# Performance work log

Hardware: AMD Instinct MI355X
Metric: run time of the kernel (lower is better)

Reference implementation:

```python
import jax, jax.numpy as jnp
import numpy as np

B, S, DIM, H = 2, 2048, 1024, 16
HD = DIM // H

def setup_inputs() -> dict:
    key = jax.random.key(0)
    ks = jax.random.split(key, 11)
    sc = DIM ** -0.5
    return {
        "q": jax.random.normal(ks[0], (B, S, DIM), jnp.float32),
        "k": jax.random.normal(ks[1], (B, S, DIM), jnp.float32),
        "v": jax.random.normal(ks[2], (B, S, DIM), jnp.float32),
        "Wq": jax.random.normal(ks[3], (DIM, DIM), jnp.float32) * sc,
        "bq": jax.random.normal(ks[4], (DIM,), jnp.float32) * 0.02,
        "Wk": jax.random.normal(ks[5], (DIM, DIM), jnp.float32) * sc,
        "bk": jax.random.normal(ks[6], (DIM,), jnp.float32) * 0.02,
        "Wv": jax.random.normal(ks[7], (DIM, DIM), jnp.float32) * sc,
        "bv": jax.random.normal(ks[8], (DIM,), jnp.float32) * 0.02,
        "Wo": jax.random.normal(ks[9], (DIM, DIM), jnp.float32) * sc,
        "bo": jax.random.normal(ks[10], (DIM,), jnp.float32) * 0.02,
    }

def reference(q, k, v, Wq, bq, Wk, bk, Wv, bv, Wo, bo):
    b, s, _ = q.shape
    qh = (q @ Wq + bq).reshape(b, s, H, HD).transpose(0, 2, 1, 3)  # [B,H,S,HD]
    kh = (k @ Wk + bk).reshape(b, s, H, HD).transpose(0, 2, 1, 3)
    vh = (v @ Wv + bv).reshape(b, s, H, HD).transpose(0, 2, 1, 3)
    scale = HD ** -0.5
    scores = jnp.einsum('bhqd,bhkd->bhqk', qh, kh) * scale  # [B,H,S,S]
    causal = jnp.triu(jnp.ones((s, s), dtype=bool), k=1)
    scores = jnp.where(causal, -jnp.inf, scores)
    attn = jax.nn.softmax(scores, axis=-1)
    out = jnp.einsum('bhqk,bhkd->bhqd', attn, vh)
    out = out.transpose(0, 2, 1, 3).reshape(b, s, DIM)
    return out @ Wo + bo
```

## Files before the change

kernel.cpp:

```cpp
#include <hip/hip_runtime.h>

#define DIM 1024
#define SEQ 2048
#define NH 16
#define HD 64
#define M_TOT 4096

typedef unsigned short u16;
typedef unsigned int u32;
typedef __attribute__((ext_vector_type(8))) short bf16x8;
typedef __attribute__((ext_vector_type(4))) float f32x4;
typedef __attribute__((ext_vector_type(4))) u32 u32x4;
typedef __attribute__((ext_vector_type(4))) u16 u16x4;

__device__ __forceinline__ u16 f2bf(float f) {
  u32 x = __builtin_bit_cast(u32, f);
  x = x + 0x7fffu + ((x >> 16) & 1u);
  return (u16)(x >> 16);
}
__device__ __forceinline__ void gload_lds16(const void* g, void* l) {
  __builtin_amdgcn_global_load_lds(
      (const __attribute__((address_space(1))) u32*)g,
      (__attribute__((address_space(3))) u32*)l, 16, 0, 0);
}

__global__ __launch_bounds__(256)
void zero_out_k(u32* __restrict__ o, int n)
{
  int i = blockIdx.x * 256 + threadIdx.x;
  if (i < n) o[i] = 0;
}

__global__ __launch_bounds__(256)
void transpose_weights(const float* __restrict__ w0, const float* __restrict__ w1,
                       const float* __restrict__ w2, const float* __restrict__ w3,
                       u16* __restrict__ wt)
{
  __shared__ u16 tile[64][72];
  int z = blockIdx.z;
  const float* W = z == 0 ? w0 : z == 1 ? w1 : z == 2 ? w2 : w3;
  u16* Wt = wt + (size_t)z * DIM * DIM;
  int k0 = blockIdx.x * 64, n0 = blockIdx.y * 64;
  int t = threadIdx.x;
#pragma unroll
  for (int it = 0; it < 4; ++it) {
    int idx = it * 256 + t;
    int lr = idx >> 4, c0 = (idx & 15) * 4;
    f32x4 v = *(const f32x4*)&W[(size_t)(k0 + lr) * DIM + n0 + c0];
    u16x4 h;
#pragma unroll
    for (int j = 0; j < 4; ++j) h[j] = f2bf(v[j]);
    *(u16x4*)&tile[lr][c0] = h;
  }
  __syncthreads();
#pragma unroll
  for (int it = 0; it < 2; ++it) {
    int idx = it * 256 + t;
    int nr = idx >> 3, c0 = (idx & 7) * 8;
    alignas(16) u16 tmp[8];
#pragma unroll
    for (int j = 0; j < 8; ++j) tmp[j] = tile[c0 + j][nr];
    *(u32x4*)&Wt[(size_t)(n0 + nr) * DIM + k0 + c0] = *(u32x4*)tmp;
  }
}

#define BM 128
#define BN 128
#define BK 32

template <bool AF32, bool OUTF32>
__device__ __forceinline__ void gemm_tile(
    const void* __restrict__ Xv, const u16* __restrict__ Wt,
    const float* __restrict__ bias, void* __restrict__ Yv,
    int bm, int bn)
{
  __shared__ u16 lA[BM * BK];
  __shared__ u16 lB[BN * BK];
  int t = threadIdx.x;
  int lane = t & 63, w = t >> 6;
  int wr = (w >> 1) * 64, wc = (w & 1) * 64;
  int rl = lane & 15, kb = (lane >> 4) * 8;

  f32x4 acc[4][4] = {};

  for (int k0 = 0; k0 < DIM; k0 += BK) {
    if (AF32) {
      const float* Xf = (const float*)Xv;
#pragma unroll
      for (int it = 0; it < 4; ++it) {
        int idx = it * 256 + t;
        int row = idx >> 3, c4 = (idx & 7) * 4;
        f32x4 v = *(const f32x4*)&Xf[(size_t)(bm + row) * DIM + k0 + c4];
        u16x4 h;
#pragma unroll
        for (int j = 0; j < 4; ++j) h[j] = f2bf(v[j]);
        *(u16x4*)&lA[row * BK + c4] = h;
      }
    } else {
      const u16* Xh = (const u16*)Xv;
#pragma unroll
      for (int r = 0; r < 2; ++r) {
        int idx = r * 256 + t;
        int row = idx >> 2, ce = (idx & 3) * 8;
        gload_lds16(Xh + (size_t)(bm + row) * DIM + k0 + ce, (char*)lA + idx * 16);
      }
    }
#pragma unroll
    for (int r = 0; r < 2; ++r) {
      int idx = r * 256 + t;
      int row = idx >> 2, ce = (idx & 3) * 8;
      gload_lds16(Wt + (size_t)(bn + row) * DIM + k0 + ce, (char*)lB + idx * 16);
    }
    __syncthreads();
    bf16x8 a[4], b[4];
#pragma unroll
    for (int m = 0; m < 4; ++m)
      a[m] = *(const bf16x8*)&lA[(wr + m * 16 + rl) * BK + kb];
#pragma unroll
    for (int n = 0; n < 4; ++n)
      b[n] = *(const bf16x8*)&lB[(wc + n * 16 + rl) * BK + kb];
#pragma unroll
    for (int m = 0; m < 4; ++m)
#pragma unroll
      for (int n = 0; n < 4; ++n)
        acc[m][n] = __builtin_amdgcn_mfma_f32_16x16x32_bf16(a[m], b[n], acc[m][n], 0, 0, 0);
    __syncthreads();
  }

  int rh = (lane >> 4) * 4;
#pragma unroll
  for (int n = 0; n < 4; ++n) {
    int col = bn + wc + n * 16 + rl;
    float bv = bias[col];
#pragma unroll
    for (int m = 0; m < 4; ++m) {
      int row = bm + wr + m * 16 + rh;
#pragma unroll
      for (int r = 0; r < 4; ++r) {
        if (OUTF32)
          ((float*)Yv)[(size_t)(row + r) * DIM + col] = acc[m][n][r] + bv;
        else
          ((u16*)Yv)[(size_t)(row + r) * DIM + col] = f2bf(acc[m][n][r] + bv);
      }
    }
  }
}

__global__ __launch_bounds__(256)
void gemm_qkv(const float* __restrict__ xq, const float* __restrict__ xk, const float* __restrict__ xv,
              const u16* __restrict__ wt,
              const float* __restrict__ bq, const float* __restrict__ bk, const float* __restrict__ bv,
              u16* __restrict__ outbase)
{
  int z = blockIdx.z;
  const float* X = z == 0 ? xq : z == 1 ? xk : xv;
  const u16* Wt = wt + (size_t)z * DIM * DIM;
  const float* bias = z == 0 ? bq : z == 1 ? bk : bv;
  u16* Y = outbase + (size_t)z * M_TOT * DIM;
  gemm_tile<true, false>(X, Wt, bias, Y, blockIdx.x * BM, blockIdx.y * BN);
}

__global__ __launch_bounds__(256)
void gemm_o(const u16* __restrict__ X, const u16* __restrict__ Wt,
            const float* __restrict__ bias, float* __restrict__ Y)
{
  gemm_tile<false, true>(X, Wt, bias, Y, blockIdx.x * BM, blockIdx.y * BN);
}

#define SC2 0.18033688011112042f

__device__ __forceinline__ void attn_compute(
    const u16 (*lK)[72], const u16 (*lVt)[72], u16 (*lPw)[72],
    bf16x8 qf0, bf16x8 qf1, bf16x8 ones,
    int rl, int hi, int kv0, int qw, bool diag,
    f32x4* oacc, f32x4& lacc)
{
  float p[4][4];
#pragma unroll
  for (int g = 0; g < 4; ++g) {
    int kvr = g * 16 + rl;
    f32x4 c = {};
    c = __builtin_amdgcn_mfma_f32_16x16x32_bf16(qf0, *(const bf16x8*)&lK[kvr][hi * 8], c, 0, 0, 0);
    c = __builtin_amdgcn_mfma_f32_16x16x32_bf16(qf1, *(const bf16x8*)&lK[kvr][32 + hi * 8], c, 0, 0, 0);
#pragma unroll
    for (int r = 0; r < 4; ++r) p[g][r] = exp2f(c[r] * SC2);
  }
  if (diag) {
#pragma unroll
    for (int g = 0; g < 4; ++g) {
      int kv_abs = kv0 + g * 16 + rl;
#pragma unroll
      for (int r = 0; r < 4; ++r)
        if (kv_abs > qw + hi * 4 + r) p[g][r] = 0.f;
    }
  }
#pragma unroll
  for (int g = 0; g < 4; ++g)
#pragma unroll
    for (int r = 0; r < 4; ++r)
      lPw[hi * 4 + r][g * 16 + rl] = f2bf(p[g][r]);
#pragma unroll
  for (int kk = 0; kk < 2; ++kk) {
    bf16x8 pf = *(const bf16x8*)&lPw[rl][kk * 32 + hi * 8];
    lacc = __builtin_amdgcn_mfma_f32_16x16x32_bf16(pf, ones, lacc, 0, 0, 0);
#pragma unroll
    for (int n = 0; n < 4; ++n) {
      bf16x8 vf = *(const bf16x8*)&lVt[n * 16 + rl][kk * 32 + hi * 8];
      oacc[n] = __builtin_amdgcn_mfma_f32_16x16x32_bf16(pf, vf, oacc[n], 0, 0, 0);
    }
  }
}

__global__ __launch_bounds__(256)
void attn_fwd(const u16* Qp, const u16* __restrict__ Kp,
              const u16* __restrict__ Vp, u16* O)
{
  __shared__ u16 lK[64][72];
  __shared__ u16 lVt[64][72];
  __shared__ u16 lP[4][16][72];

  int bh = blockIdx.y;
  int b = bh >> 4, h = bh & 15;
  int xa = blockIdx.x;
  int xb = 31 - xa;
  int t = threadIdx.x, lane = t & 63, w = t >> 6;
  int rl = lane & 15, hi = lane >> 4;
  int qa_w = xa * 64 + w * 16;
  int qb_w = xb * 64 + w * 16;

  const u16* Qb = Qp + ((size_t)b * SEQ) * DIM + h * HD;
  const u16* Kb = Kp + ((size_t)b * SEQ) * DIM + h * HD;
  const u16* Vb = Vp + ((size_t)b * SEQ) * DIM + h * HD;

  bf16x8 qa0, qa1, qb0, qb1;
  {
    const u16* qrow = Qb + (size_t)(qa_w + rl) * DIM + hi * 8;
    qa0 = *(const bf16x8*)qrow;
    qa1 = *(const bf16x8*)(qrow + 32);
    qrow = Qb + (size_t)(qb_w + rl) * DIM + hi * 8;
    qb0 = *(const bf16x8*)qrow;
    qb1 = *(const bf16x8*)(qrow + 32);
  }
  bf16x8 ones;
#pragma unroll
  for (int j = 0; j < 8; ++j) ones[j] = (short)0x3F80;

  f32x4 oA[4] = {}, oB[4] = {};
  f32x4 lAcc = {}, lBcc = {};

  int krow = t >> 3;
  int kc8 = (t & 7) * 8;
  int kvv = t & 63;
  int vd0 = (t >> 6) * 8;

  int nt = xb + 1;
  bf16x8 kr0, kr1, vr0, vr1;
  {
    const u16* Krow = Kb + kc8;
    kr0 = *(const bf16x8*)(Krow + (size_t)krow * DIM);
    kr1 = *(const bf16x8*)(Krow + (size_t)(krow + 32) * DIM);
    const u16* Vrow = Vb + (size_t)kvv * DIM + vd0;
    vr0 = *(const bf16x8*)Vrow;
    vr1 = *(const bf16x8*)(Vrow + 32);
  }

  for (int tile = 0; tile < nt; ++tile) {
    *(bf16x8*)&lK[krow][kc8] = kr0;
    *(bf16x8*)&lK[krow + 32][kc8] = kr1;
#pragma unroll
    for (int j = 0; j < 8; ++j) lVt[vd0 + j][kvv] = (u16)vr0[j];
#pragma unroll
    for (int j = 0; j < 8; ++j) lVt[vd0 + 32 + j][kvv] = (u16)vr1[j];
    __syncthreads();
    if (tile + 1 < nt) {
      size_t kv0n = (size_t)(tile + 1) * 64;
      const u16* Krow = Kb + kv0n * DIM + kc8;
      kr0 = *(const bf16x8*)(Krow + (size_t)krow * DIM);
      kr1 = *(const bf16x8*)(Krow + (size_t)(krow + 32) * DIM);
      const u16* Vrow = Vb + (kv0n + kvv) * DIM + vd0;
      vr0 = *(const bf16x8*)Vrow;
      vr1 = *(const bf16x8*)(Vrow + 32);
    }
    int kv0 = tile * 64;
    attn_compute(lK, lVt, lP[w], qb0, qb1, ones, rl, hi, kv0, qb_w, tile == xb, oB, lBcc);
    if (tile <= xa)
      attn_compute(lK, lVt, lP[w], qa0, qa1, ones, rl, hi, kv0, qa_w, tile == xa, oA, lAcc);
    __syncthreads();
  }

#pragma unroll
  for (int n = 0; n < 4; ++n) {
    int d = n * 16 + rl;
#pragma unroll
    for (int r = 0; r < 4; ++r) {
      int qq = qa_w + hi * 4 + r;
      O[((size_t)b * SEQ + qq) * DIM + h * HD + d] = f2bf(oA[n][r] / lAcc[r]);
      qq = qb_w + hi * 4 + r;
      O[((size_t)b * SEQ + qq) * DIM + h * HD + d] = f2bf(oB[n][r] / lBcc[r]);
    }
  }
}

extern "C" void kernel_launch(void* const* d_in, const int* in_sizes, int n_in,
                              void* d_out, int out_size, void* d_ws, size_t ws_size,
                              hipStream_t stream)
{
  (void)in_sizes; (void)n_in;
  const size_t MB = 1024ull * 1024ull;
  if (ws_size < 32 * MB) {
    zero_out_k<<<(out_size + 255) / 256, 256, 0, stream>>>((u32*)d_out, out_size);
    return;
  }

  u16* Wt = (u16*)d_ws;
  u16* Qp = (u16*)((char*)d_ws + 8 * MB);
  u16* Kp = (u16*)((char*)d_ws + 16 * MB);
  u16* Vp = (u16*)((char*)d_ws + 24 * MB);

  transpose_weights<<<dim3(16, 16, 4), 256, 0, stream>>>(
      (const float*)d_in[3], (const float*)d_in[5], (const float*)d_in[7],
      (const float*)d_in[9], Wt);
  gemm_qkv<<<dim3(32, 8, 3), 256, 0, stream>>>(
      (const float*)d_in[0], (const float*)d_in[1], (const float*)d_in[2], Wt,
      (const float*)d_in[4], (const float*)d_in[6], (const float*)d_in[8], Qp);
  attn_fwd<<<dim3(16, 32), 256, 0, stream>>>(Qp, Kp, Vp, Qp);
  gemm_o<<<dim3(32, 8), 256, 0, stream>>>(Qp, Wt + 3ll * DIM * DIM,
                                          (const float*)d_in[10], (float*)d_out);
}
```

Baseline: 133.1 us.

## Double-buffer GEMM tiles and interleave dual-query attention compute

The projection GEMM now double-buffers its LDS tiles and prefetches the next K-slice (including register-staged fp32 activations) during the MFMA work on the current slice. This drops one barrier per iteration. The attention kernel adds a fused dual-query path that shares the K/V fragment loads between the two query tiles and interleaves their MFMAs for more instruction-level parallelism. It also sets an occupancy hint of 2 blocks per CU. The costs are double the GEMM LDS footprint, more registers in the dual path, and the occupancy bound may force register spills.

```diff
diff --git a/kernel.cpp b/kernel.cpp
--- a/kernel.cpp
+++ b/kernel.cpp
@@ -74,57 +74,98 @@
     const float* __restrict__ bias, void* __restrict__ Yv,
     int bm, int bn)
 {
-  __shared__ u16 lA[BM * BK];
-  __shared__ u16 lB[BN * BK];
+  __shared__ u16 lA[2][BM * BK];
+  __shared__ u16 lB[2][BN * BK];
   int t = threadIdx.x;
   int lane = t & 63, w = t >> 6;
   int wr = (w >> 1) * 64, wc = (w & 1) * 64;
   int rl = lane & 15, kb = (lane >> 4) * 8;
 
+  const float* Xf = (const float*)Xv;
+  const u16* Xh = (const u16*)Xv;
+
   f32x4 acc[4][4] = {};
-
-  for (int k0 = 0; k0 < DIM; k0 += BK) {
-    if (AF32) {
-      const float* Xf = (const float*)Xv;
+  f32x4 av[4];
+
+  if (AF32) {
+#pragma unroll
+    for (int it = 0; it < 4; ++it) {
+      int idx = it * 256 + t;
+      int row = idx >> 3, c4 = (idx & 7) * 4;
+      f32x4 v = *(const f32x4*)&Xf[(size_t)(bm + row) * DIM + c4];
+      u16x4 h;
+#pragma unroll
+      for (int j = 0; j < 4; ++j) h[j] = f2bf(v[j]);
+      *(u16x4*)&lA[0][row * BK + c4] = h;
+    }
+  } else {
+#pragma unroll
+    for (int r = 0; r < 2; ++r) {
+      int idx = r * 256 + t;
+      int row = idx >> 2, ce = (idx & 3) * 8;
+      gload_lds16(Xh + (size_t)(bm + row) * DIM + ce, (char*)&lA[0][0] + idx * 16);
+    }
+  }
+#pragma unroll
+  for (int r = 0; r < 2; ++r) {
+    int idx = r * 256 + t;
+    int row = idx >> 2, ce = (idx & 3) * 8;
+    gload_lds16(Wt + (size_t)(bn + row) * DIM + ce, (char*)&lB[0][0] + idx * 16);
+  }
+
+  for (int ki = 0; ki < DIM / BK; ++ki) {
+    int cur = ki & 1, nxt = cur ^ 1;
+    __syncthreads();
+    int k1 = (ki + 1) * BK;
+    bool more = k1 < DIM;
+    if (more) {
+      if (AF32) {
+#pragma unroll
+        for (int it = 0; it < 4; ++it) {
+          int idx = it * 256 + t;
+          int row = idx >> 3, c4 = (idx & 7) * 4;
+          av[it] = *(const f32x4*)&Xf[(size_t)(bm + row) * DIM + k1 + c4];
+        }
+      } else {
+#pragma unroll
+        for (int r = 0; r < 2; ++r) {
+          int idx = r * 256 + t;
+          int row = idx >> 2, ce = (idx & 3) * 8;
+          gload_lds16(Xh + (size_t)(bm + row) * DIM + k1 + ce,
+                      (char*)&lA[nxt][0] + idx * 16);
+        }
+      }
+#pragma unroll
+      for (int r = 0; r < 2; ++r) {
+        int idx = r * 256 + t;
+        int row = idx >> 2, ce = (idx & 3) * 8;
+        gload_lds16(Wt + (size_t)(bn + row) * DIM + k1 + ce,
+                    (char*)&lB[nxt][0] + idx * 16);
+      }
+    }
+    bf16x8 a[4], b[4];
+#pragma unroll
+    for (int m = 0; m < 4; ++m)
+      a[m] = *(const bf16x8*)&lA[cur][(wr + m * 16 + rl) * BK + kb];
+#pragma unroll
+    for (int n = 0; n < 4; ++n)
+      b[n] = *(const bf16x8*)&lB[cur][(wc + n * 16 + rl) * BK + kb];
+#pragma unroll
+    for (int m = 0; m < 4; ++m)
+#pragma unroll
+      for (int n = 0; n < 4; ++n)
+        acc[m][n] = __builtin_amdgcn_mfma_f32_16x16x32_bf16(a[m], b[n], acc[m][n], 0, 0, 0);
+    if (more && AF32) {
 #pragma unroll
       for (int it = 0; it < 4; ++it) {
         int idx = it * 256 + t;
         int row = idx >> 3, c4 = (idx & 7) * 4;
-        f32x4 v = *(const f32x4*)&Xf[(size_t)(bm + row) * DIM + k0 + c4];
         u16x4 h;
 #pragma unroll
-        for (int j = 0; j < 4; ++j) h[j] = f2bf(v[j]);
-        *(u16x4*)&lA[row * BK + c4] = h;
+        for (int j = 0; j < 4; ++j) h[j] = f2bf(av[it][j]);
+        *(u16x4*)&lA[nxt][row * BK + c4] = h;
       }
-    } else {
-      const u16* Xh = (const u16*)Xv;
-#pragma unroll
-      for (int r = 0; r < 2; ++r) {
-        int idx = r * 256 + t;
-        int row = idx >> 2, ce = (idx & 3) * 8;
-        gload_lds16(Xh + (size_t)(bm + row) * DIM + k0 + ce, (char*)lA + idx * 16);
-      }
-    }
-#pragma unroll
-    for (int r = 0; r < 2; ++r) {
-      int idx = r * 256 + t;
-      int row = idx >> 2, ce = (idx & 3) * 8;
-      gload_lds16(Wt + (size_t)(bn + row) * DIM + k0 + ce, (char*)lB + idx * 16);
-    }
-    __syncthreads();
-    bf16x8 a[4], b[4];
-#pragma unroll
-    for (int m = 0; m < 4; ++m)
-      a[m] = *(const bf16x8*)&lA[(wr + m * 16 + rl) * BK + kb];
-#pragma unroll
-    for (int n = 0; n < 4; ++n)
-      b[n] = *(const bf16x8*)&lB[(wc + n * 16 + rl) * BK + kb];
-#pragma unroll
-    for (int m = 0; m < 4; ++m)
-#pragma unroll
-      for (int n = 0; n < 4; ++n)
-        acc[m][n] = __builtin_amdgcn_mfma_f32_16x16x32_bf16(a[m], b[n], acc[m][n], 0, 0, 0);
-    __syncthreads();
+    }
   }
 
   int rh = (lane >> 4) * 4;
@@ -211,13 +252,68 @@
   }
 }
 
-__global__ __launch_bounds__(256)
+__device__ __forceinline__ void attn_compute_dual(
+    const u16 (*lK)[72], const u16 (*lVt)[72],
+    u16 (*lP0)[72], u16 (*lP1)[72],
+    bf16x8 qa0, bf16x8 qa1, bf16x8 qb0, bf16x8 qb1, bf16x8 ones,
+    int rl, int hi, int kv0, int qaw, bool diagA,
+    f32x4* oA, f32x4& lA, f32x4* oB, f32x4& lB)
+{
+  float pA[4][4], pB[4][4];
+#pragma unroll
+  for (int g = 0; g < 4; ++g) {
+    int kvr = g * 16 + rl;
+    bf16x8 kf0 = *(const bf16x8*)&lK[kvr][hi * 8];
+    bf16x8 kf1 = *(const bf16x8*)&lK[kvr][32 + hi * 8];
+    f32x4 cA = {}, cB = {};
+    cA = __builtin_amdgcn_mfma_f32_16x16x32_bf16(qa0, kf0, cA, 0, 0, 0);
+    cB = __builtin_amdgcn_mfma_f32_16x16x32_bf16(qb0, kf0, cB, 0, 0, 0);
+    cA = __builtin_amdgcn_mfma_f32_16x16x32_bf16(qa1, kf1, cA, 0, 0, 0);
+    cB = __builtin_amdgcn_mfma_f32_16x16x32_bf16(qb1, kf1, cB, 0, 0, 0);
+#pragma unroll
+    for (int r = 0; r < 4; ++r) {
+      pA[g][r] = exp2f(cA[r] * SC2);
+      pB[g][r] = exp2f(cB[r] * SC2);
+    }
+  }
+  if (diagA) {
+#pragma unroll
+    for (int g = 0; g < 4; ++g) {
+      int kv_abs = kv0 + g * 16 + rl;
+#pragma unroll
+      for (int r = 0; r < 4; ++r)
+        if (kv_abs > qaw + hi * 4 + r) pA[g][r] = 0.f;
+    }
+  }
+#pragma unroll
+  for (int g = 0; g < 4; ++g)
+#pragma unroll
+    for (int r = 0; r < 4; ++r) {
+      lP0[hi * 4 + r][g * 16 + rl] = f2bf(pA[g][r]);
+      lP1[hi * 4 + r][g * 16 + rl] = f2bf(pB[g][r]);
+    }
+#pragma unroll
+  for (int kk = 0; kk < 2; ++kk) {
+    bf16x8 pfA = *(const bf16x8*)&lP0[rl][kk * 32 + hi * 8];
+    bf16x8 pfB = *(const bf16x8*)&lP1[rl][kk * 32 + hi * 8];
+    lA = __builtin_amdgcn_mfma_f32_16x16x32_bf16(pfA, ones, lA, 0, 0, 0);
+    lB = __builtin_amdgcn_mfma_f32_16x16x32_bf16(pfB, ones, lB, 0, 0, 0);
+#pragma unroll
+    for (int n = 0; n < 4; ++n) {
+      bf16x8 vf = *(const bf16x8*)&lVt[n * 16 + rl][kk * 32 + hi * 8];
+      oA[n] = __builtin_amdgcn_mfma_f32_16x16x32_bf16(pfA, vf, oA[n], 0, 0, 0);
+      oB[n] = __builtin_amdgcn_mfma_f32_16x16x32_bf16(pfB, vf, oB[n], 0, 0, 0);
+    }
+  }
+}
+
+__global__ __launch_bounds__(256, 2)
 void attn_fwd(const u16* Qp, const u16* __restrict__ Kp,
               const u16* __restrict__ Vp, u16* O)
 {
   __shared__ u16 lK[64][72];
   __shared__ u16 lVt[64][72];
-  __shared__ u16 lP[4][16][72];
+  __shared__ u16 lP[4][2][16][72];
 
   int bh = blockIdx.y;
   int b = bh >> 4, h = bh & 15;
@@ -282,9 +378,12 @@
       vr1 = *(const bf16x8*)(Vrow + 32);
     }
     int kv0 = tile * 64;
-    attn_compute(lK, lVt, lP[w], qb0, qb1, ones, rl, hi, kv0, qb_w, tile == xb, oB, lBcc);
     if (tile <= xa)
-      attn_compute(lK, lVt, lP[w], qa0, qa1, ones, rl, hi, kv0, qa_w, tile == xa, oA, lAcc);
+      attn_compute_dual(lK, lVt, lP[w][0], lP[w][1], qa0, qa1, qb0, qb1, ones,
+                        rl, hi, kv0, qa_w, tile == xa, oA, lAcc, oB, lBcc);
+    else
+      attn_compute(lK, lVt, lP[w][0], qb0, qb1, ones,
+                   rl, hi, kv0, qb_w, tile == xb, oB, lBcc);
     __syncthreads();
   }
 
```

After: 144.0 us. +8.2%, slower.

## Double-buffer GEMM tile loads in LDS to overlap loads with MFMA

Applied to the files above, without the earlier changes.

Switches the projection GEMM's LDS tiles to two buffers. The next K-slice is prefetched (global_load_lds for bf16 inputs, register loads for fp32 inputs) while MFMAs run on the current slice, and fp32 data is converted to bf16 and stored after the compute. This removes one barrier per iteration and hides global load latency. In exchange it doubles LDS use and adds registers for the prefetched fp32 values, which may lower occupancy.

```diff
diff --git a/kernel.cpp b/kernel.cpp
--- a/kernel.cpp
+++ b/kernel.cpp
@@ -74,57 +74,98 @@
     const float* __restrict__ bias, void* __restrict__ Yv,
     int bm, int bn)
 {
-  __shared__ u16 lA[BM * BK];
-  __shared__ u16 lB[BN * BK];
+  __shared__ u16 lA[2][BM * BK];
+  __shared__ u16 lB[2][BN * BK];
   int t = threadIdx.x;
   int lane = t & 63, w = t >> 6;
   int wr = (w >> 1) * 64, wc = (w & 1) * 64;
   int rl = lane & 15, kb = (lane >> 4) * 8;
 
+  const float* Xf = (const float*)Xv;
+  const u16* Xh = (const u16*)Xv;
+
   f32x4 acc[4][4] = {};
-
-  for (int k0 = 0; k0 < DIM; k0 += BK) {
-    if (AF32) {
-      const float* Xf = (const float*)Xv;
+  f32x4 av[4];
+
+  if (AF32) {
+#pragma unroll
+    for (int it = 0; it < 4; ++it) {
+      int idx = it * 256 + t;
+      int row = idx >> 3, c4 = (idx & 7) * 4;
+      f32x4 v = *(const f32x4*)&Xf[(size_t)(bm + row) * DIM + c4];
+      u16x4 h;
+#pragma unroll
+      for (int j = 0; j < 4; ++j) h[j] = f2bf(v[j]);
+      *(u16x4*)&lA[0][row * BK + c4] = h;
+    }
+  } else {
+#pragma unroll
+    for (int r = 0; r < 2; ++r) {
+      int idx = r * 256 + t;
+      int row = idx >> 2, ce = (idx & 3) * 8;
+      gload_lds16(Xh + (size_t)(bm + row) * DIM + ce, (char*)&lA[0][0] + idx * 16);
+    }
+  }
+#pragma unroll
+  for (int r = 0; r < 2; ++r) {
+    int idx = r * 256 + t;
+    int row = idx >> 2, ce = (idx & 3) * 8;
+    gload_lds16(Wt + (size_t)(bn + row) * DIM + ce, (char*)&lB[0][0] + idx * 16);
+  }
+
+  for (int ki = 0; ki < DIM / BK; ++ki) {
+    int cur = ki & 1, nxt = cur ^ 1;
+    __syncthreads();
+    int k1 = (ki + 1) * BK;
+    bool more = k1 < DIM;
+    if (more) {
+      if (AF32) {
+#pragma unroll
+        for (int it = 0; it < 4; ++it) {
+          int idx = it * 256 + t;
+          int row = idx >> 3, c4 = (idx & 7) * 4;
+          av[it] = *(const f32x4*)&Xf[(size_t)(bm + row) * DIM + k1 + c4];
+        }
+      } else {
+#pragma unroll
+        for (int r = 0; r < 2; ++r) {
+          int idx = r * 256 + t;
+          int row = idx >> 2, ce = (idx & 3) * 8;
+          gload_lds16(Xh + (size_t)(bm + row) * DIM + k1 + ce,
+                      (char*)&lA[nxt][0] + idx * 16);
+        }
+      }
+#pragma unroll
+      for (int r = 0; r < 2; ++r) {
+        int idx = r * 256 + t;
+        int row = idx >> 2, ce = (idx & 3) * 8;
+        gload_lds16(Wt + (size_t)(bn + row) * DIM + k1 + ce,
+                    (char*)&lB[nxt][0] + idx * 16);
+      }
+    }
+    bf16x8 a[4], b[4];
+#pragma unroll
+    for (int m = 0; m < 4; ++m)
+      a[m] = *(const bf16x8*)&lA[cur][(wr + m * 16 + rl) * BK + kb];
+#pragma unroll
+    for (int n = 0; n < 4; ++n)
+      b[n] = *(const bf16x8*)&lB[cur][(wc + n * 16 + rl) * BK + kb];
+#pragma unroll
+    for (int m = 0; m < 4; ++m)
+#pragma unroll
+      for (int n = 0; n < 4; ++n)
+        acc[m][n] = __builtin_amdgcn_mfma_f32_16x16x32_bf16(a[m], b[n], acc[m][n], 0, 0, 0);
+    if (more && AF32) {
 #pragma unroll
       for (int it = 0; it < 4; ++it) {
         int idx = it * 256 + t;
         int row = idx >> 3, c4 = (idx & 7) * 4;
-        f32x4 v = *(const f32x4*)&Xf[(size_t)(bm + row) * DIM + k0 + c4];
         u16x4 h;
 #pragma unroll
-        for (int j = 0; j < 4; ++j) h[j] = f2bf(v[j]);
-        *(u16x4*)&lA[row * BK + c4] = h;
+        for (int j = 0; j < 4; ++j) h[j] = f2bf(av[it][j]);
+        *(u16x4*)&lA[nxt][row * BK + c4] = h;
       }
-    } else {
-      const u16* Xh = (const u16*)Xv;
-#pragma unroll
-      for (int r = 0; r < 2; ++r) {
-        int idx = r * 256 + t;
-        int row = idx >> 2, ce = (idx & 3) * 8;
-        gload_lds16(Xh + (size_t)(bm + row) * DIM + k0 + ce, (char*)lA + idx * 16);
-      }
-    }
-#pragma unroll
-    for (int r = 0; r < 2; ++r) {
-      int idx = r * 256 + t;
-      int row = idx >> 2, ce = (idx & 3) * 8;
-      gload_lds16(Wt + (size_t)(bn + row) * DIM + k0 + ce, (char*)lB + idx * 16);
-    }
-    __syncthreads();
-    bf16x8 a[4], b[4];
-#pragma unroll
-    for (int m = 0; m < 4; ++m)
-      a[m] = *(const bf16x8*)&lA[(wr + m * 16 + rl) * BK + kb];
-#pragma unroll
-    for (int n = 0; n < 4; ++n)
-      b[n] = *(const bf16x8*)&lB[(wc + n * 16 + rl) * BK + kb];
-#pragma unroll
-    for (int m = 0; m < 4; ++m)
-#pragma unroll
-      for (int n = 0; n < 4; ++n)
-        acc[m][n] = __builtin_amdgcn_mfma_f32_16x16x32_bf16(a[m], b[n], acc[m][n], 0, 0, 0);
-    __syncthreads();
+    }
   }
 
   int rh = (lane >> 4) * 4;
```

After: 138.2 us. 3.8% more time.

## Switch attention to 32x32x16 MFMA with 32-row warp tiles and paired query blocks

Applied to the files above, without the earlier changes.

Rewrites the attention inner step to use 32x32x16 bf16 MFMAs, so each wave handles 32 query rows instead of 16. Each block now covers two near/far 64-row query tile pairs across its four waves, which halves the grid to 8x32 blocks and doubles how many query rows reuse each K/V tile staged in LDS. The aim is fewer K/V global loads and LDS fills per query row, plus better MFMA throughput. The cost is that waves in a block now have unequal tile counts, so some idle through the shared tile loop, and the grid has fewer blocks, which lowers occupancy and parallelism.

```diff
diff --git a/kernel.cpp b/kernel.cpp
--- a/kernel.cpp
+++ b/kernel.cpp
@@ -10,6 +10,7 @@
 typedef unsigned int u32;
 typedef __attribute__((ext_vector_type(8))) short bf16x8;
 typedef __attribute__((ext_vector_type(4))) float f32x4;
+typedef __attribute__((ext_vector_type(16))) float f32x16;
 typedef __attribute__((ext_vector_type(4))) u32 u32x4;
 typedef __attribute__((ext_vector_type(4))) u16 u16x4;
 
@@ -169,45 +170,41 @@
 
 #define SC2 0.18033688011112042f
 
-__device__ __forceinline__ void attn_compute(
+__device__ __forceinline__ void attn_compute32(
     const u16 (*lK)[72], const u16 (*lVt)[72], u16 (*lPw)[72],
-    bf16x8 qf0, bf16x8 qf1, bf16x8 ones,
-    int rl, int hi, int kv0, int qw, bool diag,
-    f32x4* oacc, f32x4& lacc)
-{
-  float p[4][4];
-#pragma unroll
-  for (int g = 0; g < 4; ++g) {
-    int kvr = g * 16 + rl;
-    f32x4 c = {};
-    c = __builtin_amdgcn_mfma_f32_16x16x32_bf16(qf0, *(const bf16x8*)&lK[kvr][hi * 8], c, 0, 0, 0);
-    c = __builtin_amdgcn_mfma_f32_16x16x32_bf16(qf1, *(const bf16x8*)&lK[kvr][32 + hi * 8], c, 0, 0, 0);
-#pragma unroll
-    for (int r = 0; r < 4; ++r) p[g][r] = exp2f(c[r] * SC2);
-  }
-  if (diag) {
-#pragma unroll
-    for (int g = 0; g < 4; ++g) {
-      int kv_abs = kv0 + g * 16 + rl;
-#pragma unroll
-      for (int r = 0; r < 4; ++r)
-        if (kv_abs > qw + hi * 4 + r) p[g][r] = 0.f;
-    }
-  }
-#pragma unroll
-  for (int g = 0; g < 4; ++g)
-#pragma unroll
-    for (int r = 0; r < 4; ++r)
-      lPw[hi * 4 + r][g * 16 + rl] = f2bf(p[g][r]);
-#pragma unroll
-  for (int kk = 0; kk < 2; ++kk) {
-    bf16x8 pf = *(const bf16x8*)&lPw[rl][kk * 32 + hi * 8];
-    lacc = __builtin_amdgcn_mfma_f32_16x16x32_bf16(pf, ones, lacc, 0, 0, 0);
-#pragma unroll
-    for (int n = 0; n < 4; ++n) {
-      bf16x8 vf = *(const bf16x8*)&lVt[n * 16 + rl][kk * 32 + hi * 8];
-      oacc[n] = __builtin_amdgcn_mfma_f32_16x16x32_bf16(pf, vf, oacc[n], 0, 0, 0);
-    }
+    const bf16x8* qf, bf16x8 ones,
+    int l31, int h5, int kv0, int qbase, bool diag,
+    f32x16& o0, f32x16& o1, f32x16& lacc)
+{
+  f32x16 sa = {}, sb = {};
+#pragma unroll
+  for (int ds = 0; ds < 4; ++ds) {
+    bf16x8 ka = *(const bf16x8*)&lK[l31][ds * 16 + h5 * 8];
+    bf16x8 kb = *(const bf16x8*)&lK[32 + l31][ds * 16 + h5 * 8];
+    sa = __builtin_amdgcn_mfma_f32_32x32x16_bf16(qf[ds], ka, sa, 0, 0, 0);
+    sb = __builtin_amdgcn_mfma_f32_32x32x16_bf16(qf[ds], kb, sb, 0, 0, 0);
+  }
+#pragma unroll
+  for (int r = 0; r < 16; ++r) {
+    int lq = (r & 3) + 8 * (r >> 2) + 4 * h5;
+    float pa = exp2f(sa[r] * SC2);
+    float pb = exp2f(sb[r] * SC2);
+    if (diag) {
+      int qrow = qbase + lq;
+      if (kv0 + l31 > qrow) pa = 0.f;
+      if (kv0 + 32 + l31 > qrow) pb = 0.f;
+    }
+    lPw[lq][l31] = f2bf(pa);
+    lPw[lq][32 + l31] = f2bf(pb);
+  }
+#pragma unroll
+  for (int ks = 0; ks < 4; ++ks) {
+    bf16x8 pf = *(const bf16x8*)&lPw[l31][ks * 16 + h5 * 8];
+    lacc = __builtin_amdgcn_mfma_f32_32x32x16_bf16(pf, ones, lacc, 0, 0, 0);
+    bf16x8 va = *(const bf16x8*)&lVt[l31][ks * 16 + h5 * 8];
+    bf16x8 vb = *(const bf16x8*)&lVt[32 + l31][ks * 16 + h5 * 8];
+    o0 = __builtin_amdgcn_mfma_f32_32x32x16_bf16(pf, va, o0, 0, 0, 0);
+    o1 = __builtin_amdgcn_mfma_f32_32x32x16_bf16(pf, vb, o1, 0, 0, 0);
   }
 }
 
@@ -217,43 +214,44 @@
 {
   __shared__ u16 lK[64][72];
   __shared__ u16 lVt[64][72];
-  __shared__ u16 lP[4][16][72];
+  __shared__ u16 lP[4][32][72];
 
   int bh = blockIdx.y;
   int b = bh >> 4, h = bh & 15;
-  int xa = blockIdx.x;
-  int xb = 31 - xa;
+  int bx = blockIdx.x;
   int t = threadIdx.x, lane = t & 63, w = t >> 6;
-  int rl = lane & 15, hi = lane >> 4;
-  int qa_w = xa * 64 + w * 16;
-  int qb_w = xb * 64 + w * 16;
+  int l31 = lane & 31, h5 = lane >> 5;
+
+  int p_near = 2 * bx + (w >> 1);
+  int p_far = 31 - p_near;
+  int rowoff = (w & 1) * 32;
+  int qn_base = p_near * 64 + rowoff;
+  int qf_base = p_far * 64 + rowoff;
+  int nt_w = p_far + 1;
+  int nt_max = 32 - 2 * bx;
 
   const u16* Qb = Qp + ((size_t)b * SEQ) * DIM + h * HD;
   const u16* Kb = Kp + ((size_t)b * SEQ) * DIM + h * HD;
   const u16* Vb = Vp + ((size_t)b * SEQ) * DIM + h * HD;
 
-  bf16x8 qa0, qa1, qb0, qb1;
-  {
-    const u16* qrow = Qb + (size_t)(qa_w + rl) * DIM + hi * 8;
-    qa0 = *(const bf16x8*)qrow;
-    qa1 = *(const bf16x8*)(qrow + 32);
-    qrow = Qb + (size_t)(qb_w + rl) * DIM + hi * 8;
-    qb0 = *(const bf16x8*)qrow;
-    qb1 = *(const bf16x8*)(qrow + 32);
+  bf16x8 qN[4], qF[4];
+#pragma unroll
+  for (int ds = 0; ds < 4; ++ds) {
+    qN[ds] = *(const bf16x8*)(Qb + (size_t)(qn_base + l31) * DIM + ds * 16 + h5 * 8);
+    qF[ds] = *(const bf16x8*)(Qb + (size_t)(qf_base + l31) * DIM + ds * 16 + h5 * 8);
   }
   bf16x8 ones;
 #pragma unroll
   for (int j = 0; j < 8; ++j) ones[j] = (short)0x3F80;
 
-  f32x4 oA[4] = {}, oB[4] = {};
-  f32x4 lAcc = {}, lBcc = {};
+  f32x16 oN0 = {}, oN1 = {}, oF0 = {}, oF1 = {};
+  f32x16 lN = {}, lF = {};
 
   int krow = t >> 3;
   int kc8 = (t & 7) * 8;
   int kvv = t & 63;
   int vd0 = (t >> 6) * 8;
 
-  int nt = xb + 1;
   bf16x8 kr0, kr1, vr0, vr1;
   {
     const u16* Krow = Kb + kc8;
@@ -264,7 +262,7 @@
     vr1 = *(const bf16x8*)(Vrow + 32);
   }
 
-  for (int tile = 0; tile < nt; ++tile) {
+  for (int tile = 0; tile < nt_max; ++tile) {
     *(bf16x8*)&lK[krow][kc8] = kr0;
     *(bf16x8*)&lK[krow + 32][kc8] = kr1;
 #pragma unroll
@@ -272,7 +270,7 @@
 #pragma unroll
     for (int j = 0; j < 8; ++j) lVt[vd0 + 32 + j][kvv] = (u16)vr1[j];
     __syncthreads();
-    if (tile + 1 < nt) {
+    if (tile + 1 < nt_max) {
       size_t kv0n = (size_t)(tile + 1) * 64;
       const u16* Krow = Kb + kv0n * DIM + kc8;
       kr0 = *(const bf16x8*)(Krow + (size_t)krow * DIM);
@@ -282,22 +280,24 @@
       vr1 = *(const bf16x8*)(Vrow + 32);
     }
     int kv0 = tile * 64;
-    attn_compute(lK, lVt, lP[w], qb0, qb1, ones, rl, hi, kv0, qb_w, tile == xb, oB, lBcc);
-    if (tile <= xa)
-      attn_compute(lK, lVt, lP[w], qa0, qa1, ones, rl, hi, kv0, qa_w, tile == xa, oA, lAcc);
+    if (tile < nt_w)
+      attn_compute32(lK, lVt, lP[w], qF, ones, l31, h5, kv0, qf_base,
+                     tile == p_far, oF0, oF1, lF);
+    if (tile <= p_near)
+      attn_compute32(lK, lVt, lP[w], qN, ones, l31, h5, kv0, qn_base,
+                     tile == p_near, oN0, oN1, lN);
     __syncthreads();
   }
 
 #pragma unroll
-  for (int n = 0; n < 4; ++n) {
-    int d = n * 16 + rl;
-#pragma unroll
-    for (int r = 0; r < 4; ++r) {
-      int qq = qa_w + hi * 4 + r;
-      O[((size_t)b * SEQ + qq) * DIM + h * HD + d] = f2bf(oA[n][r] / lAcc[r]);
-      qq = qb_w + hi * 4 + r;
-      O[((size_t)b * SEQ + qq) * DIM + h * HD + d] = f2bf(oB[n][r] / lBcc[r]);
-    }
+  for (int r = 0; r < 16; ++r) {
+    int lq = (r & 3) + 8 * (r >> 2) + 4 * h5;
+    size_t rowN = ((size_t)b * SEQ + qn_base + lq) * DIM + h * HD;
+    size_t rowF = ((size_t)b * SEQ + qf_base + lq) * DIM + h * HD;
+    O[rowN + l31] = f2bf(oN0[r] / lN[r]);
+    O[rowN + 32 + l31] = f2bf(oN1[r] / lN[r]);
+    O[rowF + l31] = f2bf(oF0[r] / lF[r]);
+    O[rowF + 32 + l31] = f2bf(oF1[r] / lF[r]);
   }
 }
 
@@ -323,7 +323,7 @@
   gemm_qkv<<<dim3(32, 8, 3), 256, 0, stream>>>(
       (const float*)d_in[0], (const float*)d_in[1], (const float*)d_in[2], Wt,
       (const float*)d_in[4], (const float*)d_in[6], (const float*)d_in[8], Qp);
-  attn_fwd<<<dim3(16, 32), 256, 0, stream>>>(Qp, Kp, Vp, Qp);
+  attn_fwd<<<dim3(8, 32), 256, 0, stream>>>(Qp, Kp, Vp, Qp);
   gemm_o<<<dim3(32, 8), 256, 0, stream>>>(Qp, Wt + 3ll * DIM * DIM,
                                           (const float*)d_in[10], (float*)d_out);
 }
```

Result: slower. 156.5 us (+17.6%).
